# Optimization experiments

Measured on AMD Instinct MI355X. Metric: run time of the kernel, lower is better.

The kernel has to match this reference:

```python
import jax, jax.numpy as jnp
import numpy as np

B, H, N = 256, 128, 1000

def setup_inputs() -> dict:
    key = jax.random.key(0)
    k1, k2, k3, k4, k5, k6 = jax.random.split(key, 6)
    return {
        "adj_hidden": jax.random.normal(k1, (B, H, N), dtype=jnp.float32),
        "static_hidden": jax.random.normal(k2, (B, H, N), dtype=jnp.float32),
        "dynamic_hidden": jax.random.normal(k3, (B, H, N), dtype=jnp.float32),
        "decoder_hidden": jax.random.normal(k4, (B, H), dtype=jnp.float32),
        "v": jax.random.normal(k5, (1, 1, H), dtype=jnp.float32) * 0.1,
        "W": jax.random.normal(k6, (1, H, 4 * H), dtype=jnp.float32) * 0.05,
    }

def reference(adj_hidden, static_hidden, dynamic_hidden, decoder_hidden, v, W):
    # hidden: [B, 4H, N] -- decoder_hidden broadcast along node dim
    dec = jnp.broadcast_to(decoder_hidden[:, :, None], static_hidden.shape)
    hidden = jnp.concatenate((adj_hidden, static_hidden, dynamic_hidden, dec), axis=1)
    # W[0]: [H, 4H]; scores: [B, H, N]
    Wh = jnp.tanh(jnp.einsum('hk,bkn->bhn', W[0], hidden))
    # v[0,0]: [H]; attns: [B, 1, N]
    attns = jnp.einsum('h,bhn->bn', v[0, 0], Wh)[:, None, :]
    return jax.nn.softmax(attns, axis=2)
```

## Files before the change

### kernel.cpp

```cpp
#include <hip/hip_runtime.h>
#include <hip/hip_bf16.h>
#include <cstdint>


#define BB 256
#define HH 128
#define NN 1000
#define K3 384
#define WROW 784
#define WLDS (HH * WROW)
#define CT_OFF WLDS
#define VV_OFF (WLDS + 512)
#define SMEM_ATTN (WLDS + 1024)

typedef __attribute__((ext_vector_type(8))) short short8;
typedef __attribute__((ext_vector_type(4))) float f32x4;

__device__ __forceinline__ uint32_t pk_bf16_rn(float a, float b) {
    union { __hip_bfloat162 h2; uint32_t u; } cv;
    cv.h2 = __float22bfloat162_rn(make_float2(a, b));
    return cv.u;
}
__device__ __forceinline__ float fast_tanh(float x) {
    float e = __expf(2.0f * x);
    return 1.0f - 2.0f * __builtin_amdgcn_rcpf(e + 1.0f);
}

__global__ void prep_kernel(const float* __restrict__ W, const float* __restrict__ dec,
                            uint16_t* __restrict__ Whi, float* __restrict__ cterm) {
    extern __shared__ float ls[];
    const int tid = threadIdx.x;
    if (blockIdx.x < 48) {
        int idx4 = blockIdx.x * 256 + tid;
        int h = idx4 / 96, k4 = idx4 - h * 96;
        float4 w = *(const float4*)(W + h * 512 + k4 * 4);
        uint2 o;
        o.x = pk_bf16_rn(w.x, w.y);
        o.y = pk_bf16_rn(w.z, w.w);
        *(uint2*)(Whi + h * K3 + k4 * 4) = o;
    } else {
        float* w4 = ls;
        float* dl = ls + 128 * 129;
        const int bb = (blockIdx.x - 48) * 8;
#pragma unroll
        for (int i = 0; i < 16; ++i) {
            int chunk = tid + i * 256;
            int h = chunk >> 5, kq = chunk & 31;
            float4 v = *(const float4*)(W + h * 512 + 384 + kq * 4);
            float* d = w4 + h * 129 + kq * 4;
            d[0] = v.x; d[1] = v.y; d[2] = v.z; d[3] = v.w;
        }
        {
            float4 dv = *(const float4*)(dec + bb * HH + tid * 4);
            float* d = dl + tid * 4;
            d[0] = dv.x; d[1] = dv.y; d[2] = dv.z; d[3] = dv.w;
        }
        __syncthreads();
#pragma unroll
        for (int r = 0; r < 4; ++r) {
            int o = tid + r * 256;
            int h = o & 127, bl_ = o >> 7;
            const float* wr = w4 + h * 129;
            const float* dr = dl + bl_ * 128;
            float s = 0.f;
#pragma unroll 8
            for (int k = 0; k < 128; ++k) s += wr[k] * dr[k];
            cterm[(bb + bl_) * HH + h] = s;
        }
    }
}

__launch_bounds__(1024, 4)
__global__ void attn_main(const float* __restrict__ adj, const float* __restrict__ sta,
                          const float* __restrict__ dyn,
                          const uint16_t* __restrict__ Whi,
                          const float* __restrict__ cterm, const float* __restrict__ vvec,
                          float* __restrict__ logits) {
    extern __shared__ char smem[];
    const int tid = threadIdx.x;
    const int b = blockIdx.x >> 2;
    const int tile = blockIdx.x & 3;

#pragma unroll
    for (int i = 0; i < 6; ++i) {
        int ch = tid + i * 1024;
        int h = ch / 48, j = ch - h * 48;
        *(uint4*)(smem + h * WROW + j * 16) = *(const uint4*)(Whi + h * K3 + j * 8);
    }
    if (tid < 32) {
        ((float4*)(smem + CT_OFF))[tid] = ((const float4*)(cterm + b * HH))[tid];
    } else if (tid < 64) {
        ((float4*)(smem + VV_OFF))[tid - 32] = ((const float4*)vvec)[tid - 32];
    }
    __syncthreads();

    const int wave = tid >> 6, lane = tid & 63;
    const int c = lane & 15, q = lane >> 4;
    const int n = tile * 256 + wave * 16 + c;
    const int ncl = (n < NN) ? n : NN - 1;
    const long bbase = (long)b * HH * NN;
    const float* A0 = adj + bbase;
    const float* A1 = sta + bbase;
    const float* A2 = dyn + bbase;

    f32x4 acc[8];
#pragma unroll
    for (int m = 0; m < 8; ++m) acc[m] = (f32x4){0.f, 0.f, 0.f, 0.f};

    union fu { uint32_t u[4]; short8 s; };

    float x[8], xn[8];
    {
        const float* p = A0 + (8 * q) * NN + ncl;
#pragma unroll
        for (int j = 0; j < 8; ++j) x[j] = p[j * NN];
    }

#pragma unroll
    for (int it = 0; it < 12; ++it) {
        if (it + 1 < 12) {
            const int t2 = (it + 1) >> 2, cc2 = (it + 1) & 3;
            const float* base2 = (t2 == 0) ? A0 : ((t2 == 1) ? A1 : A2);
            const float* p = base2 + (cc2 * 32 + 8 * q) * NN + ncl;
#pragma unroll
            for (int j = 0; j < 8; ++j) xn[j] = p[j * NN];
        }
        fu bh, bl;
#pragma unroll
        for (int j = 0; j < 4; ++j) {
            float a = x[2 * j], d = x[2 * j + 1];
            uint32_t u = pk_bf16_rn(a, d);
            bh.u[j] = u;
            float la = a - __uint_as_float(u << 16);
            float lb = d - __uint_as_float(u & 0xFFFF0000u);
            bl.u[j] = pk_bf16_rn(la, lb);
        }
        const int rowoff = (it >> 2) * 256 + (it & 3) * 64 + q * 16;
#pragma unroll
        for (int m = 0; m < 8; ++m) {
            const short8 av = *(const short8*)(smem + (m * 16 + c) * WROW + rowoff);
            acc[m] = __builtin_amdgcn_mfma_f32_16x16x32_bf16(av, bh.s, acc[m], 0, 0, 0);
            acc[m] = __builtin_amdgcn_mfma_f32_16x16x32_bf16(av, bl.s, acc[m], 0, 0, 0);
        }
        if (it + 1 < 12) {
#pragma unroll
            for (int j = 0; j < 8; ++j) x[j] = xn[j];
        }
    }

    const float* ct = (const float*)(smem + CT_OFF);
    const float* vv = (const float*)(smem + VV_OFF);
    float s = 0.0f;
#pragma unroll
    for (int m = 0; m < 8; ++m) {
#pragma unroll
        for (int r = 0; r < 4; ++r) {
            const int h = m * 16 + q * 4 + r;
            s += vv[h] * fast_tanh(acc[m][r] + ct[h]);
        }
    }
    s += __shfl_xor(s, 16, 64);
    s += __shfl_xor(s, 32, 64);
    if (lane < 16 && n < NN) logits[b * NN + n] = s;
}

__global__ void softmax_kernel(float* __restrict__ out) {
    const int b = blockIdx.x;
    const int tid = threadIdx.x;
    float* row = out + b * NN;

    float vals[4];
#pragma unroll
    for (int i = 0; i < 4; ++i) {
        int j = tid + i * 256;
        vals[i] = (j < NN) ? row[j] : -1e30f;
    }
    float mx = fmaxf(fmaxf(vals[0], vals[1]), fmaxf(vals[2], vals[3]));
#pragma unroll
    for (int off = 1; off < 64; off <<= 1) mx = fmaxf(mx, __shfl_xor(mx, off, 64));
    __shared__ float smax[4];
    if ((tid & 63) == 0) smax[tid >> 6] = mx;
    __syncthreads();
    mx = fmaxf(fmaxf(smax[0], smax[1]), fmaxf(smax[2], smax[3]));

    float e[4];
    float s = 0.0f;
#pragma unroll
    for (int i = 0; i < 4; ++i) {
        int j = tid + i * 256;
        e[i] = (j < NN) ? __expf(vals[i] - mx) : 0.0f;
        s += e[i];
    }
#pragma unroll
    for (int off = 1; off < 64; off <<= 1) s += __shfl_xor(s, off, 64);
    __shared__ float ssum[4];
    if ((tid & 63) == 0) ssum[tid >> 6] = s;
    __syncthreads();
    s = ssum[0] + ssum[1] + ssum[2] + ssum[3];
    float inv = 1.0f / s;
#pragma unroll
    for (int i = 0; i < 4; ++i) {
        int j = tid + i * 256;
        if (j < NN) row[j] = e[i] * inv;
    }
}

extern "C" void kernel_launch(void* const* d_in, const int* in_sizes, int n_in,
                              void* d_out, int out_size, void* d_ws, size_t ws_size,
                              hipStream_t stream) {
    const float* adj = (const float*)d_in[0];
    const float* sta = (const float*)d_in[1];
    const float* dyn = (const float*)d_in[2];
    const float* dec = (const float*)d_in[3];
    const float* v   = (const float*)d_in[4];
    const float* W   = (const float*)d_in[5];

    uint16_t* Whi = (uint16_t*)d_ws;
    float* cterm  = (float*)(Whi + HH * K3);
    float* logits = (float*)d_out;

    prep_kernel<<<80, 256, (128 * 129 + 1024) * 4, stream>>>(W, dec, Whi, cterm);
    attn_main<<<BB * 4, 1024, SMEM_ATTN, stream>>>(adj, sta, dyn, Whi, cterm, v, logits);
    softmax_kernel<<<BB, 256, 0, stream>>>(logits);
}
```

Before: 368.6 us.

## Switch to single fp16 MFMA pass and stage W in two K-halves

```diff
diff --git a/kernel.cpp b/kernel.cpp
--- a/kernel.cpp
+++ b/kernel.cpp
@@ -1,5 +1,5 @@
 #include <hip/hip_runtime.h>
-#include <hip/hip_bf16.h>
+#include <hip/hip_fp16.h>
 #include <cstdint>
 
 
@@ -7,19 +7,19 @@
 #define HH 128
 #define NN 1000
 #define K3 384
-#define WROW 784
+#define KH 192
+#define WROW 400
 #define WLDS (HH * WROW)
 #define CT_OFF WLDS
 #define VV_OFF (WLDS + 512)
 #define SMEM_ATTN (WLDS + 1024)
 
-typedef __attribute__((ext_vector_type(8))) short short8;
+typedef __attribute__((ext_vector_type(8))) _Float16 half8;
 typedef __attribute__((ext_vector_type(4))) float f32x4;
 
-__device__ __forceinline__ uint32_t pk_bf16_rn(float a, float b) {
-    union { __hip_bfloat162 h2; uint32_t u; } cv;
-    cv.h2 = __float22bfloat162_rn(make_float2(a, b));
-    return cv.u;
+__device__ __forceinline__ uint32_t pk_f16(float a, float b) {
+    auto h = __builtin_amdgcn_cvt_pkrtz(a, b);
+    return __builtin_bit_cast(uint32_t, h);
 }
 __device__ __forceinline__ float fast_tanh(float x) {
     float e = __expf(2.0f * x);
@@ -27,17 +27,19 @@
 }
 
 __global__ void prep_kernel(const float* __restrict__ W, const float* __restrict__ dec,
-                            uint16_t* __restrict__ Whi, float* __restrict__ cterm) {
+                            uint16_t* __restrict__ Whf, float* __restrict__ cterm) {
     extern __shared__ float ls[];
     const int tid = threadIdx.x;
     if (blockIdx.x < 48) {
         int idx4 = blockIdx.x * 256 + tid;
         int h = idx4 / 96, k4 = idx4 - h * 96;
         float4 w = *(const float4*)(W + h * 512 + k4 * 4);
-        uint2 o;
-        o.x = pk_bf16_rn(w.x, w.y);
-        o.y = pk_bf16_rn(w.z, w.w);
-        *(uint2*)(Whi + h * K3 + k4 * 4) = o;
+        union { __half hx[4]; uint2 u; } o;
+        o.hx[0] = __float2half_rn(w.x);
+        o.hx[1] = __float2half_rn(w.y);
+        o.hx[2] = __float2half_rn(w.z);
+        o.hx[3] = __float2half_rn(w.w);
+        *(uint2*)(Whf + h * K3 + k4 * 4) = o.u;
     } else {
         float* w4 = ls;
         float* dl = ls + 128 * 129;
@@ -70,33 +72,20 @@
     }
 }
 
-__launch_bounds__(1024, 4)
+__launch_bounds__(512, 6)
 __global__ void attn_main(const float* __restrict__ adj, const float* __restrict__ sta,
                           const float* __restrict__ dyn,
-                          const uint16_t* __restrict__ Whi,
+                          const uint16_t* __restrict__ Whf,
                           const float* __restrict__ cterm, const float* __restrict__ vvec,
                           float* __restrict__ logits) {
     extern __shared__ char smem[];
     const int tid = threadIdx.x;
-    const int b = blockIdx.x >> 2;
-    const int tile = blockIdx.x & 3;
-
-#pragma unroll
-    for (int i = 0; i < 6; ++i) {
-        int ch = tid + i * 1024;
-        int h = ch / 48, j = ch - h * 48;
-        *(uint4*)(smem + h * WROW + j * 16) = *(const uint4*)(Whi + h * K3 + j * 8);
-    }
-    if (tid < 32) {
-        ((float4*)(smem + CT_OFF))[tid] = ((const float4*)(cterm + b * HH))[tid];
-    } else if (tid < 64) {
-        ((float4*)(smem + VV_OFF))[tid - 32] = ((const float4*)vvec)[tid - 32];
-    }
-    __syncthreads();
+    const int b = blockIdx.x >> 3;
+    const int tile = blockIdx.x & 7;
 
     const int wave = tid >> 6, lane = tid & 63;
     const int c = lane & 15, q = lane >> 4;
-    const int n = tile * 256 + wave * 16 + c;
+    const int n = tile * 128 + wave * 16 + c;
     const int ncl = (n < NN) ? n : NN - 1;
     const long bbase = (long)b * HH * NN;
     const float* A0 = adj + bbase;
@@ -107,44 +96,58 @@
 #pragma unroll
     for (int m = 0; m < 8; ++m) acc[m] = (f32x4){0.f, 0.f, 0.f, 0.f};
 
-    union fu { uint32_t u[4]; short8 s; };
-
-    float x[8], xn[8];
+    union bu { uint32_t u[4]; half8 h; };
+    bu bcur;
+
     {
-        const float* p = A0 + (8 * q) * NN + ncl;
-#pragma unroll
-        for (int j = 0; j < 8; ++j) x[j] = p[j * NN];
-    }
-
-#pragma unroll
-    for (int it = 0; it < 12; ++it) {
-        if (it + 1 < 12) {
-            const int t2 = (it + 1) >> 2, cc2 = (it + 1) & 3;
-            const float* base2 = (t2 == 0) ? A0 : ((t2 == 1) ? A1 : A2);
-            const float* p = base2 + (cc2 * 32 + 8 * q) * NN + ncl;
-#pragma unroll
-            for (int j = 0; j < 8; ++j) xn[j] = p[j * NN];
-        }
-        fu bh, bl;
-#pragma unroll
-        for (int j = 0; j < 4; ++j) {
-            float a = x[2 * j], d = x[2 * j + 1];
-            uint32_t u = pk_bf16_rn(a, d);
-            bh.u[j] = u;
-            float la = a - __uint_as_float(u << 16);
-            float lb = d - __uint_as_float(u & 0xFFFF0000u);
-            bl.u[j] = pk_bf16_rn(la, lb);
-        }
-        const int rowoff = (it >> 2) * 256 + (it & 3) * 64 + q * 16;
-#pragma unroll
-        for (int m = 0; m < 8; ++m) {
-            const short8 av = *(const short8*)(smem + (m * 16 + c) * WROW + rowoff);
-            acc[m] = __builtin_amdgcn_mfma_f32_16x16x32_bf16(av, bh.s, acc[m], 0, 0, 0);
-            acc[m] = __builtin_amdgcn_mfma_f32_16x16x32_bf16(av, bl.s, acc[m], 0, 0, 0);
-        }
-        if (it + 1 < 12) {
-#pragma unroll
-            for (int j = 0; j < 8; ++j) x[j] = xn[j];
+        const float* px = A0 + (8 * q) * NN + ncl;
+        float x0[8];
+#pragma unroll
+        for (int j = 0; j < 8; ++j) x0[j] = px[j * NN];
+#pragma unroll
+        for (int j = 0; j < 4; ++j) bcur.u[j] = pk_f16(x0[2 * j], x0[2 * j + 1]);
+    }
+
+#pragma unroll
+    for (int pp = 0; pp < 2; ++pp) {
+        if (pp) __syncthreads();
+#pragma unroll
+        for (int i = 0; i < 6; ++i) {
+            int ch = tid + i * 512;
+            int hr = ch / 24, j = ch - hr * 24;
+            *(uint4*)(smem + hr * WROW + j * 16) =
+                *(const uint4*)(Whf + hr * K3 + pp * KH + j * 8);
+        }
+        if (pp == 0) {
+            if (tid < 32) {
+                ((float4*)(smem + CT_OFF))[tid] = ((const float4*)(cterm + b * HH))[tid];
+            } else if (tid < 64) {
+                ((float4*)(smem + VV_OFF))[tid - 32] = ((const float4*)vvec)[tid - 32];
+            }
+        }
+        __syncthreads();
+
+#pragma unroll
+        for (int it = 0; it < 6; ++it) {
+            const int kk = pp * 6 + it;
+            float xf[8];
+            if (kk + 1 < 12) {
+                const int t2 = (kk + 1) >> 2, cc2 = (kk + 1) & 3;
+                const float* base2 = (t2 == 0) ? A0 : ((t2 == 1) ? A1 : A2);
+                const float* px = base2 + (cc2 * 32 + 8 * q) * NN + ncl;
+#pragma unroll
+                for (int j = 0; j < 8; ++j) xf[j] = px[j * NN];
+            }
+            const int rowoff = it * 64 + q * 16;
+#pragma unroll
+            for (int m = 0; m < 8; ++m) {
+                const half8 av = *(const half8*)(smem + (m * 16 + c) * WROW + rowoff);
+                acc[m] = __builtin_amdgcn_mfma_f32_16x16x32_f16(av, bcur.h, acc[m], 0, 0, 0);
+            }
+            if (kk + 1 < 12) {
+#pragma unroll
+                for (int j = 0; j < 4; ++j) bcur.u[j] = pk_f16(xf[2 * j], xf[2 * j + 1]);
+            }
         }
     }
 
@@ -215,11 +218,11 @@
     const float* v   = (const float*)d_in[4];
     const float* W   = (const float*)d_in[5];
 
-    uint16_t* Whi = (uint16_t*)d_ws;
-    float* cterm  = (float*)(Whi + HH * K3);
+    uint16_t* Whf = (uint16_t*)d_ws;
+    float* cterm  = (float*)(Whf + HH * K3);
     float* logits = (float*)d_out;
 
-    prep_kernel<<<80, 256, (128 * 129 + 1024) * 4, stream>>>(W, dec, Whi, cterm);
-    attn_main<<<BB * 4, 1024, SMEM_ATTN, stream>>>(adj, sta, dyn, Whi, cterm, v, logits);
+    prep_kernel<<<80, 256, (128 * 129 + 1024) * 4, stream>>>(W, dec, Whf, cterm);
+    attn_main<<<BB * 8, 512, SMEM_ATTN, stream>>>(adj, sta, dyn, Whf, cterm, v, logits);
     softmax_kernel<<<BB, 256, 0, stream>>>(logits);
 }
```

Measured after the change: 360.1 us. 2.3% less time.
